# Kernel tuning notes

Hardware: AMD Instinct MI355X
Metric: run time of the kernel (lower is better)

The kernel has to match this reference:

```python
import math
import jax, jax.numpy as jnp
import numpy as np

B, S, D, H = 1, 4096, 1024, 16
HD = D // H


def setup_inputs() -> dict:
    key = jax.random.key(0)
    ks = jax.random.split(key, 11)
    s = 0.02
    inp = {
        "q": jax.random.normal(ks[0], (B, S, D), jnp.float32),
        "k": jax.random.normal(ks[1], (B, S, D), jnp.float32),
        "v": jax.random.normal(ks[2], (B, S, D), jnp.float32),
        # causal boolean mask, broadcastable over [B, H, S, S]
        "mask": jnp.tril(jnp.ones((S, S), jnp.bool_))[None, None],
        "Wq": jax.random.normal(ks[3], (D, D), jnp.float32) * s,
        "bq": jnp.zeros((D,), jnp.float32),
        "Wk": jax.random.normal(ks[4], (D, D), jnp.float32) * s,
        "bk": jnp.zeros((D,), jnp.float32),
        "Wv": jax.random.normal(ks[5], (D, D), jnp.float32) * s,
        "bv": jnp.zeros((D,), jnp.float32),
        "Wo": jax.random.normal(ks[6], (D, D), jnp.float32) * s,
        "bo": jnp.zeros((D,), jnp.float32),
    }
    return inp


def reference(q, k, v, mask, Wq, bq, Wk, bk, Wv, bv, Wo, bo):
    # projections (torch Linear: x @ W.T + b; here W is stored already transposed)
    qp = (q @ Wq + bq).reshape(B, S, H, HD)
    kp = (k @ Wk + bk).reshape(B, S, H, HD)
    vp = (v @ Wv + bv).reshape(B, S, H, HD)
    # scores: [B, H, S, S]
    scores = jnp.einsum("bqhd,bkhd->bhqk", qp, kp) / math.sqrt(HD)
    scores = jnp.where(mask, scores, -jnp.inf)
    attn = jax.nn.softmax(scores, axis=-1)
    # context: [B, H, S, HD] -> [B, S, D]
    ctx = jnp.einsum("bhqk,bkhd->bqhd", attn, vp).reshape(B, S, D)
    return ctx @ Wo + bo
```

## Files before the change

kernel.cpp:

```cpp
#include <hip/hip_runtime.h>
#include <hip/hip_bf16.h>


#define S_LEN 4096
#define D_DIM 1024
#define NHEAD 16
#define HDIM  64

typedef __hip_bfloat16 bf16;
typedef __attribute__((ext_vector_type(8))) short bf16x8v;
typedef __attribute__((ext_vector_type(4))) float f32x4;

#define MFMA16(a, b, c) __builtin_amdgcn_mfma_f32_16x16x32_bf16((a), (b), (c), 0, 0, 0)

__device__ __forceinline__ void async_cp16(const void* g, void* l) {
    __builtin_amdgcn_global_load_lds(
        (const __attribute__((address_space(1))) unsigned int*)g,
        (__attribute__((address_space(3))) unsigned int*)l, 16, 0, 0);
}

__global__ __launch_bounds__(256) void cvt_bf16_k(
    const float* __restrict__ x0, const float* __restrict__ x1,
    const float* __restrict__ x2,
    bf16* __restrict__ y0, bf16* __restrict__ y1, bf16* __restrict__ y2)
{
    const float* x = (blockIdx.z == 0) ? x0 : (blockIdx.z == 1) ? x1 : x2;
    bf16*       y = (blockIdx.z == 0) ? y0 : (blockIdx.z == 1) ? y1 : y2;
    const size_t i = ((size_t)blockIdx.x * 256 + threadIdx.x);
    const float4 v = ((const float4*)x)[i];
    union { bf16 h[4]; short4 s; } u;
    u.h[0] = __float2bfloat16(v.x);
    u.h[1] = __float2bfloat16(v.y);
    u.h[2] = __float2bfloat16(v.z);
    u.h[3] = __float2bfloat16(v.w);
    ((short4*)y)[i] = u.s;
}

__global__ __launch_bounds__(256) void transpose_cvt_k(
    const float* __restrict__ W0, const float* __restrict__ W1,
    const float* __restrict__ W2, const float* __restrict__ W3,
    bf16* __restrict__ T0, bf16* __restrict__ T1,
    bf16* __restrict__ T2, bf16* __restrict__ T3)
{
    const float* W = (blockIdx.z == 0) ? W0 : (blockIdx.z == 1) ? W1
                   : (blockIdx.z == 2) ? W2 : W3;
    bf16*       Wt = (blockIdx.z == 0) ? T0 : (blockIdx.z == 1) ? T1
                   : (blockIdx.z == 2) ? T2 : T3;
    __shared__ float t[32][33];
    const int bx = blockIdx.x << 5, by = blockIdx.y << 5;
    const int tx = threadIdx.x & 31, ty = threadIdx.x >> 5;
#pragma unroll
    for (int i = 0; i < 32; i += 8)
        t[ty + i][tx] = W[(size_t)(by + ty + i) * D_DIM + bx + tx];
    __syncthreads();
#pragma unroll
    for (int i = 0; i < 32; i += 8)
        Wt[(size_t)(bx + ty + i) * D_DIM + by + tx] = __float2bfloat16(t[tx][ty + i]);
}

struct GemmJob {
    const bf16* A; const bf16* Wt; const float* bias; void* out;
    int mode; float scale;
};

__global__ __launch_bounds__(256) void gemm_k(GemmJob j0, GemmJob j1, GemmJob j2)
{
    const GemmJob j = (blockIdx.z == 0) ? j0 : (blockIdx.z == 1) ? j1 : j2;
    const int K = D_DIM;
    const int bn = blockIdx.x << 6;
    const int bm = blockIdx.y << 7;
    const int tid = threadIdx.x;
    const int w = tid >> 6, lane = tid & 63;
    const int col = lane & 15, g = lane >> 4;
    const int wr = (w >> 1) << 6, wc = (w & 1) << 5;

    __shared__ bf16 As[128 * 64];
    __shared__ bf16 Bs[64 * 64];

    f32x4 acc[4][2];
#pragma unroll
    for (int i = 0; i < 4; ++i)
#pragma unroll
        for (int jj = 0; jj < 2; ++jj) acc[i][jj] = (f32x4){0.f, 0.f, 0.f, 0.f};

    for (int kb = 0; kb < K; kb += 64) {
        __syncthreads();
#pragma unroll
        for (int e = 0; e < 4; ++e) {
            const int lin = (e << 8) + tid;
            const int row = lin >> 3, kc = lin & 7;
            async_cp16(j.A + (size_t)(bm + row) * K + kb + (kc << 3), &As[lin << 3]);
        }
#pragma unroll
        for (int e = 0; e < 2; ++e) {
            const int lin = (e << 8) + tid;
            const int row = lin >> 3, kc = lin & 7;
            async_cp16(j.Wt + (size_t)(bn + row) * K + kb + (kc << 3), &Bs[lin << 3]);
        }
        __syncthreads();

#pragma unroll
        for (int s = 0; s < 2; ++s) {
            bf16x8v af[4], bfv[2];
#pragma unroll
            for (int i = 0; i < 4; ++i)
                af[i] = *(const bf16x8v*)&As[((wr + (i << 4) + col) << 6) + (s << 5) + (g << 3)];
#pragma unroll
            for (int jj = 0; jj < 2; ++jj)
                bfv[jj] = *(const bf16x8v*)&Bs[((wc + (jj << 4) + col) << 6) + (s << 5) + (g << 3)];
#pragma unroll
            for (int i = 0; i < 4; ++i)
#pragma unroll
                for (int jj = 0; jj < 2; ++jj)
                    acc[i][jj] = MFMA16(af[i], bfv[jj], acc[i][jj]);
        }
    }

#pragma unroll
    for (int i = 0; i < 4; ++i)
#pragma unroll
    for (int jj = 0; jj < 2; ++jj)
#pragma unroll
    for (int reg = 0; reg < 4; ++reg) {
        const int row = bm + wr + (i << 4) + (g << 2) + reg;
        const int cg  = bn + wc + (jj << 4) + col;
        const float vv = (acc[i][jj][reg] + j.bias[cg]) * j.scale;
        if (j.mode == 0)
            ((bf16*)j.out)[(((size_t)(cg >> 6)) * S_LEN + row) * HDIM + (cg & 63)] =
                __float2bfloat16(vv);
        else if (j.mode == 2)
            ((bf16*)j.out)[((size_t)(cg >> 6) * HDIM + (cg & 63)) * S_LEN + row] =
                __float2bfloat16(vv);
        else
            ((float*)j.out)[(size_t)row * D_DIM + cg] = vv;
    }
}

__global__ __launch_bounds__(256) void attn_mfma_k(
    const bf16* __restrict__ Qp, const bf16* __restrict__ Kp,
    const bf16* __restrict__ Vt, bf16* __restrict__ ctx)
{
    __shared__ bf16 Ks[4096];
    __shared__ bf16 Vs[4096];
    __shared__ bf16 Ps[4][1024];

    const int bid = blockIdx.x;
    const int qb  = 63 - (bid >> 4);
    const int h   = bid & 15;
    const int q0  = qb << 6;
    const int tid = threadIdx.x, w = tid >> 6, lane = tid & 63;
    const int col = lane & 15, g = lane >> 4;

    const bf16* Kh = Kp + (size_t)h * S_LEN * HDIM;
    const bf16* Vh = Vt + (size_t)h * HDIM * S_LEN;

    const size_t qrow_base = ((size_t)h * S_LEN + q0 + (w << 4) + col) * HDIM + (g << 3);
    const bf16x8v qf0 = *(const bf16x8v*)(Qp + qrow_base);
    const bf16x8v qf1 = *(const bf16x8v*)(Qp + qrow_base + 32);

    const int sig_r = (col >> 2) | (((col & 3) ^ (g & 1)) << 2);
    const int pr0 = (((g) << 4) | sig_r) << 3;
    const int pr1 = (((4 + g) << 4) | sig_r) << 3;
    int pw[4][4];
#pragma unroll
    for (int t = 0; t < 4; ++t) {
        const int Gw = (t << 1) + (col >> 3);
#pragma unroll
        for (int reg = 0; reg < 4; ++reg) {
            const int sig = g | (((reg ^ (Gw & 1)) & 3) << 2);
            pw[t][reg] = (((Gw << 4) | sig) << 3) + (col & 7);
        }
    }

    float pl[4] = {0.f, 0.f, 0.f, 0.f};
    f32x4 acco[4];
#pragma unroll
    for (int t = 0; t < 4; ++t) acco[t] = (f32x4){0.f, 0.f, 0.f, 0.f};

    const int nkb = qb + 1;
    for (int kb = 0; kb < nkb; ++kb) {
        const int kk0 = kb << 6;
        __syncthreads();
#pragma unroll
        for (int e = 0; e < 2; ++e) {
            const int lin = (e << 8) + tid;
            const int t = lin >> 7, G = (lin >> 4) & 7, c = lin & 15;
            async_cp16(Kh + (size_t)(kk0 + (t << 4) + c) * HDIM + (G << 3),
                       &Ks[lin << 3]);
            async_cp16(Vh + (size_t)((t << 4) + c) * S_LEN + kk0 + (G << 3),
                       &Vs[lin << 3]);
        }
        __syncthreads();

        f32x4 sa[4];
#pragma unroll
        for (int t = 0; t < 4; ++t) sa[t] = (f32x4){0.f, 0.f, 0.f, 0.f};
#pragma unroll
        for (int t = 0; t < 4; ++t) {
            sa[t] = MFMA16(qf0, *(const bf16x8v*)&Ks[((t << 7) + (g << 4) + col) << 3], sa[t]);
            sa[t] = MFMA16(qf1, *(const bf16x8v*)&Ks[((t << 7) + 64 + (g << 4) + col) << 3], sa[t]);
        }

        const bool lastt = (kb == nkb - 1);
#pragma unroll
        for (int t = 0; t < 4; ++t) {
#pragma unroll
            for (int reg = 0; reg < 4; ++reg) {
                float p;
                if (lastt && (kk0 + (t << 4) + col > q0 + (w << 4) + (g << 2) + reg))
                    p = 0.f;
                else
                    p = __expf(sa[t][reg]);
                pl[reg] += p;
                Ps[w][pw[t][reg]] = __float2bfloat16(p);
            }
        }

        const bf16x8v pf0 = *(const bf16x8v*)&Ps[w][pr0];
        const bf16x8v pf1 = *(const bf16x8v*)&Ps[w][pr1];
#pragma unroll
        for (int t = 0; t < 4; ++t) {
            acco[t] = MFMA16(pf0, *(const bf16x8v*)&Vs[((t << 7) + (g << 4) + col) << 3], acco[t]);
            acco[t] = MFMA16(pf1, *(const bf16x8v*)&Vs[((t << 7) + 64 + (g << 4) + col) << 3], acco[t]);
        }
    }

    float lrow[4];
#pragma unroll
    for (int reg = 0; reg < 4; ++reg) {
        float l = pl[reg];
        l += __shfl_xor(l, 1);
        l += __shfl_xor(l, 2);
        l += __shfl_xor(l, 4);
        l += __shfl_xor(l, 8);
        lrow[reg] = l;
    }

#pragma unroll
    for (int t = 0; t < 4; ++t)
#pragma unroll
        for (int reg = 0; reg < 4; ++reg) {
            const int row = q0 + (w << 4) + (g << 2) + reg;
            ctx[(size_t)row * D_DIM + h * HDIM + (t << 4) + col] =
                __float2bfloat16(acco[t][reg] / lrow[reg]);
        }
}

extern "C" void kernel_launch(void* const* d_in, const int* in_sizes, int n_in,
                              void* d_out, int out_size, void* d_ws, size_t ws_size,
                              hipStream_t stream)
{
    const float* q  = (const float*)d_in[0];
    const float* k  = (const float*)d_in[1];
    const float* v  = (const float*)d_in[2];
    const float* Wq = (const float*)d_in[4];
    const float* bq = (const float*)d_in[5];
    const float* Wk = (const float*)d_in[6];
    const float* bk = (const float*)d_in[7];
    const float* Wv = (const float*)d_in[8];
    const float* bv = (const float*)d_in[9];
    const float* Wo = (const float*)d_in[10];
    const float* bo = (const float*)d_in[11];

    const size_t PE  = (size_t)S_LEN * D_DIM;
    const size_t WTE = (size_t)D_DIM * D_DIM;

    const dim3 tg(32, 32, 4);
    const dim3 gg(D_DIM / 64, S_LEN / 128, 1);
    const dim3 gg3(D_DIM / 64, S_LEN / 128, 3);
    const dim3 cg((unsigned)(PE / 1024), 1, 3);

    if (ws_size >= (size_t)64 * 1024 * 1024) {
        bf16* Qb = (bf16*)d_ws;
        bf16* Kb = Qb + PE;
        bf16* Vb = Kb + PE;
        bf16* Qp = Vb + PE;
        bf16* Kp = Qp + PE;
        bf16* Vt = Kp + PE;
        bf16* Wtq = Vt + PE;
        bf16* Wtk = Wtq + WTE;
        bf16* Wtv = Wtk + WTE;
        bf16* Wto = Wtv + WTE;
        bf16* ctx = Qb;

        transpose_cvt_k<<<tg, 256, 0, stream>>>(Wq, Wk, Wv, Wo, Wtq, Wtk, Wtv, Wto);
        cvt_bf16_k<<<cg, 256, 0, stream>>>(q, k, v, Qb, Kb, Vb);

        GemmJob jq{Qb, Wtq, bq, Qp, 0, 0.125f};
        GemmJob jk{Kb, Wtk, bk, Kp, 0, 1.0f};
        GemmJob jv{Vb, Wtv, bv, Vt, 2, 1.0f};
        gemm_k<<<gg3, 256, 0, stream>>>(jq, jk, jv);

        attn_mfma_k<<<dim3(1024), 256, 0, stream>>>(Qp, Kp, Vt, ctx);

        GemmJob jo{ctx, Wto, bo, d_out, 1, 1.0f};
        gemm_k<<<gg, 256, 0, stream>>>(jo, jo, jo);
    } else {
        bf16* X  = (bf16*)d_ws;
        bf16* Qp = X + PE;
        bf16* Kp = Qp + PE;
        bf16* Vt = Kp + PE;
        bf16* Wtq = Vt + PE;
        bf16* Wtk = Wtq + WTE;
        bf16* Wtv = Wtk + WTE;
        bf16* Wto = Wtv + WTE;

        transpose_cvt_k<<<tg, 256, 0, stream>>>(Wq, Wk, Wv, Wo, Wtq, Wtk, Wtv, Wto);

        const dim3 cg1((unsigned)(PE / 1024), 1, 1);
        cvt_bf16_k<<<cg1, 256, 0, stream>>>(q, q, q, X, X, X);
        GemmJob jq{X, Wtq, bq, Qp, 0, 0.125f};
        gemm_k<<<gg, 256, 0, stream>>>(jq, jq, jq);
        cvt_bf16_k<<<cg1, 256, 0, stream>>>(k, k, k, X, X, X);
        GemmJob jk{X, Wtk, bk, Kp, 0, 1.0f};
        gemm_k<<<gg, 256, 0, stream>>>(jk, jk, jk);
        cvt_bf16_k<<<cg1, 256, 0, stream>>>(v, v, v, X, X, X);
        GemmJob jv{X, Wtv, bv, Vt, 2, 1.0f};
        gemm_k<<<gg, 256, 0, stream>>>(jv, jv, jv);

        attn_mfma_k<<<dim3(1024), 256, 0, stream>>>(Qp, Kp, Vt, X);

        GemmJob jo{X, Wto, bo, d_out, 1, 1.0f};
        gemm_k<<<gg, 256, 0, stream>>>(jo, jo, jo);
    }
}
```

Measured before the change: 324.3 us.

## Enlarge GEMM tiles with swizzled LDS, double-buffer attention K/V, use exp2

```diff
diff --git a/kernel.cpp b/kernel.cpp
--- a/kernel.cpp
+++ b/kernel.cpp
@@ -9,14 +9,20 @@
 
 typedef __hip_bfloat16 bf16;
 typedef __attribute__((ext_vector_type(8))) short bf16x8v;
+typedef __attribute__((ext_vector_type(4))) short bf16x4v;
 typedef __attribute__((ext_vector_type(4))) float f32x4;
 
 #define MFMA16(a, b, c) __builtin_amdgcn_mfma_f32_16x16x32_bf16((a), (b), (c), 0, 0, 0)
+#define LOG2E 1.44269504088896340736f
 
 __device__ __forceinline__ void async_cp16(const void* g, void* l) {
     __builtin_amdgcn_global_load_lds(
         (const __attribute__((address_space(1))) unsigned int*)g,
         (__attribute__((address_space(3))) unsigned int*)l, 16, 0, 0);
+}
+
+__device__ __forceinline__ short bf_bits(float x) {
+    union { bf16 h; short s; } u; u.h = __float2bfloat16(x); return u.s;
 }
 
 __global__ __launch_bounds__(256) void cvt_bf16_k(
@@ -67,51 +73,51 @@
 {
     const GemmJob j = (blockIdx.z == 0) ? j0 : (blockIdx.z == 1) ? j1 : j2;
     const int K = D_DIM;
-    const int bn = blockIdx.x << 6;
+    const int bn = blockIdx.x << 7;
     const int bm = blockIdx.y << 7;
     const int tid = threadIdx.x;
     const int w = tid >> 6, lane = tid & 63;
     const int col = lane & 15, g = lane >> 4;
-    const int wr = (w >> 1) << 6, wc = (w & 1) << 5;
+    const int wr = (w >> 1) << 6, wc = (w & 1) << 6;
 
     __shared__ bf16 As[128 * 64];
-    __shared__ bf16 Bs[64 * 64];
-
-    f32x4 acc[4][2];
+    __shared__ bf16 Bs[128 * 64];
+
+    f32x4 acc[4][4];
 #pragma unroll
     for (int i = 0; i < 4; ++i)
 #pragma unroll
-        for (int jj = 0; jj < 2; ++jj) acc[i][jj] = (f32x4){0.f, 0.f, 0.f, 0.f};
+        for (int jj = 0; jj < 4; ++jj) acc[i][jj] = (f32x4){0.f, 0.f, 0.f, 0.f};
 
     for (int kb = 0; kb < K; kb += 64) {
         __syncthreads();
 #pragma unroll
         for (int e = 0; e < 4; ++e) {
             const int lin = (e << 8) + tid;
-            const int row = lin >> 3, kc = lin & 7;
-            async_cp16(j.A + (size_t)(bm + row) * K + kb + (kc << 3), &As[lin << 3]);
-        }
-#pragma unroll
-        for (int e = 0; e < 2; ++e) {
-            const int lin = (e << 8) + tid;
-            const int row = lin >> 3, kc = lin & 7;
-            async_cp16(j.Wt + (size_t)(bn + row) * K + kb + (kc << 3), &Bs[lin << 3]);
+            const int row = lin >> 3, kcs = lin & 7;
+            const int kcg = kcs ^ (row & 7);
+            async_cp16(j.A  + (size_t)(bm + row) * K + kb + (kcg << 3), &As[lin << 3]);
+            async_cp16(j.Wt + (size_t)(bn + row) * K + kb + (kcg << 3), &Bs[lin << 3]);
         }
         __syncthreads();
 
 #pragma unroll
         for (int s = 0; s < 2; ++s) {
-            bf16x8v af[4], bfv[2];
+            bf16x8v af[4], bfv[4];
+#pragma unroll
+            for (int i = 0; i < 4; ++i) {
+                const int row = wr + (i << 4) + col;
+                af[i] = *(const bf16x8v*)&As[(((row << 3) + (((s << 2) + g) ^ (row & 7)))) << 3];
+            }
+#pragma unroll
+            for (int jj = 0; jj < 4; ++jj) {
+                const int row = wc + (jj << 4) + col;
+                bfv[jj] = *(const bf16x8v*)&Bs[(((row << 3) + (((s << 2) + g) ^ (row & 7)))) << 3];
+            }
 #pragma unroll
             for (int i = 0; i < 4; ++i)
-                af[i] = *(const bf16x8v*)&As[((wr + (i << 4) + col) << 6) + (s << 5) + (g << 3)];
-#pragma unroll
-            for (int jj = 0; jj < 2; ++jj)
-                bfv[jj] = *(const bf16x8v*)&Bs[((wc + (jj << 4) + col) << 6) + (s << 5) + (g << 3)];
-#pragma unroll
-            for (int i = 0; i < 4; ++i)
-#pragma unroll
-                for (int jj = 0; jj < 2; ++jj)
+#pragma unroll
+                for (int jj = 0; jj < 4; ++jj)
                     acc[i][jj] = MFMA16(af[i], bfv[jj], acc[i][jj]);
         }
     }
@@ -119,7 +125,7 @@
 #pragma unroll
     for (int i = 0; i < 4; ++i)
 #pragma unroll
-    for (int jj = 0; jj < 2; ++jj)
+    for (int jj = 0; jj < 4; ++jj)
 #pragma unroll
     for (int reg = 0; reg < 4; ++reg) {
         const int row = bm + wr + (i << 4) + (g << 2) + reg;
@@ -140,8 +146,8 @@
     const bf16* __restrict__ Qp, const bf16* __restrict__ Kp,
     const bf16* __restrict__ Vt, bf16* __restrict__ ctx)
 {
-    __shared__ bf16 Ks[4096];
-    __shared__ bf16 Vs[4096];
+    __shared__ bf16 Ks[2][4096];
+    __shared__ bf16 Vs[2][4096];
     __shared__ bf16 Ps[4][1024];
 
     const int bid = blockIdx.x;
@@ -158,83 +164,85 @@
     const bf16x8v qf0 = *(const bf16x8v*)(Qp + qrow_base);
     const bf16x8v qf1 = *(const bf16x8v*)(Qp + qrow_base + 32);
 
-    const int sig_r = (col >> 2) | (((col & 3) ^ (g & 1)) << 2);
-    const int pr0 = (((g) << 4) | sig_r) << 3;
-    const int pr1 = (((4 + g) << 4) | sig_r) << 3;
-    int pw[4][4];
-#pragma unroll
-    for (int t = 0; t < 4; ++t) {
-        const int Gw = (t << 1) + (col >> 3);
-#pragma unroll
-        for (int reg = 0; reg < 4; ++reg) {
-            const int sig = g | (((reg ^ (Gw & 1)) & 3) << 2);
-            pw[t][reg] = (((Gw << 4) | sig) << 3) + (col & 7);
-        }
-    }
-
-    float pl[4] = {0.f, 0.f, 0.f, 0.f};
+    float pl = 0.f;
     f32x4 acco[4];
 #pragma unroll
     for (int t = 0; t < 4; ++t) acco[t] = (f32x4){0.f, 0.f, 0.f, 0.f};
 
     const int nkb = qb + 1;
+
+#pragma unroll
+    for (int e = 0; e < 2; ++e) {
+        const int lin = (e << 8) + tid;
+        const int t = lin >> 7, G = (lin >> 4) & 7, c = lin & 15;
+        async_cp16(Kh + (size_t)((t << 4) + c) * HDIM + (G << 3), &Ks[0][lin << 3]);
+        async_cp16(Vh + (size_t)((t << 4) + c) * S_LEN + (G << 3), &Vs[0][lin << 3]);
+    }
+
     for (int kb = 0; kb < nkb; ++kb) {
         const int kk0 = kb << 6;
         __syncthreads();
-#pragma unroll
-        for (int e = 0; e < 2; ++e) {
-            const int lin = (e << 8) + tid;
-            const int t = lin >> 7, G = (lin >> 4) & 7, c = lin & 15;
-            async_cp16(Kh + (size_t)(kk0 + (t << 4) + c) * HDIM + (G << 3),
-                       &Ks[lin << 3]);
-            async_cp16(Vh + (size_t)((t << 4) + c) * S_LEN + kk0 + (G << 3),
-                       &Vs[lin << 3]);
-        }
-        __syncthreads();
+        if (kb + 1 < nkb) {
+            const int nk0 = (kb + 1) << 6;
+            const int nb  = (kb + 1) & 1;
+#pragma unroll
+            for (int e = 0; e < 2; ++e) {
+                const int lin = (e << 8) + tid;
+                const int t = lin >> 7, G = (lin >> 4) & 7, c = lin & 15;
+                async_cp16(Kh + (size_t)(nk0 + (t << 4) + c) * HDIM + (G << 3),
+                           &Ks[nb][lin << 3]);
+                async_cp16(Vh + (size_t)((t << 4) + c) * S_LEN + nk0 + (G << 3),
+                           &Vs[nb][lin << 3]);
+            }
+        }
+        const bf16* K0 = Ks[kb & 1];
+        const bf16* V0 = Vs[kb & 1];
 
         f32x4 sa[4];
 #pragma unroll
         for (int t = 0; t < 4; ++t) sa[t] = (f32x4){0.f, 0.f, 0.f, 0.f};
 #pragma unroll
         for (int t = 0; t < 4; ++t) {
-            sa[t] = MFMA16(qf0, *(const bf16x8v*)&Ks[((t << 7) + (g << 4) + col) << 3], sa[t]);
-            sa[t] = MFMA16(qf1, *(const bf16x8v*)&Ks[((t << 7) + 64 + (g << 4) + col) << 3], sa[t]);
+            const bf16x8v kf0 = *(const bf16x8v*)&K0[((t << 7) + (g << 4) + col) << 3];
+            const bf16x8v kf1 = *(const bf16x8v*)&K0[((t << 7) + 64 + (g << 4) + col) << 3];
+            sa[t] = MFMA16(kf0, qf0, sa[t]);
+            sa[t] = MFMA16(kf1, qf1, sa[t]);
         }
 
         const bool lastt = (kb == nkb - 1);
+        const int qq = (w << 4) + col;
 #pragma unroll
         for (int t = 0; t < 4; ++t) {
+            float p[4];
 #pragma unroll
             for (int reg = 0; reg < 4; ++reg) {
-                float p;
-                if (lastt && (kk0 + (t << 4) + col > q0 + (w << 4) + (g << 2) + reg))
-                    p = 0.f;
-                else
-                    p = __expf(sa[t][reg]);
-                pl[reg] += p;
-                Ps[w][pw[t][reg]] = __float2bfloat16(p);
+                const int krel = (t << 4) + (g << 2) + reg;
+                p[reg] = (lastt && krel > qq) ? 0.f
+                       : __builtin_amdgcn_exp2f(sa[t][reg]);
             }
-        }
-
-        const bf16x8v pf0 = *(const bf16x8v*)&Ps[w][pr0];
-        const bf16x8v pf1 = *(const bf16x8v*)&Ps[w][pr1];
+            pl += (p[0] + p[1]) + (p[2] + p[3]);
+            bf16x4v pv = { bf_bits(p[0]), bf_bits(p[1]), bf_bits(p[2]), bf_bits(p[3]) };
+            const int off = (((((t << 1) + (g >> 1)) << 4) + col) << 3) + ((g & 1) << 2);
+            *(bf16x4v*)&Ps[w][off] = pv;
+        }
+
+        const bf16x8v pf0 = *(const bf16x8v*)&Ps[w][((g << 4) + col) << 3];
+        const bf16x8v pf1 = *(const bf16x8v*)&Ps[w][(((4 + g) << 4) + col) << 3];
 #pragma unroll
         for (int t = 0; t < 4; ++t) {
-            acco[t] = MFMA16(pf0, *(const bf16x8v*)&Vs[((t << 7) + (g << 4) + col) << 3], acco[t]);
-            acco[t] = MFMA16(pf1, *(const bf16x8v*)&Vs[((t << 7) + 64 + (g << 4) + col) << 3], acco[t]);
-        }
-    }
-
-    float lrow[4];
-#pragma unroll
-    for (int reg = 0; reg < 4; ++reg) {
-        float l = pl[reg];
-        l += __shfl_xor(l, 1);
-        l += __shfl_xor(l, 2);
-        l += __shfl_xor(l, 4);
-        l += __shfl_xor(l, 8);
-        lrow[reg] = l;
-    }
+            const bf16x8v vf0 = *(const bf16x8v*)&V0[((t << 7) + (g << 4) + col) << 3];
+            const bf16x8v vf1 = *(const bf16x8v*)&V0[((t << 7) + 64 + (g << 4) + col) << 3];
+            acco[t] = MFMA16(pf0, vf0, acco[t]);
+            acco[t] = MFMA16(pf1, vf1, acco[t]);
+        }
+    }
+
+    float l = pl;
+    l += __shfl_xor(l, 16);
+    l += __shfl_xor(l, 32);
+    float lr[4];
+#pragma unroll
+    for (int reg = 0; reg < 4; ++reg) lr[reg] = __shfl(l, (g << 2) + reg);
 
 #pragma unroll
     for (int t = 0; t < 4; ++t)
@@ -242,7 +250,7 @@
         for (int reg = 0; reg < 4; ++reg) {
             const int row = q0 + (w << 4) + (g << 2) + reg;
             ctx[(size_t)row * D_DIM + h * HDIM + (t << 4) + col] =
-                __float2bfloat16(acco[t][reg] / lrow[reg]);
+                __float2bfloat16(acco[t][reg] / lr[reg]);
         }
 }
 
@@ -264,10 +272,11 @@
 
     const size_t PE  = (size_t)S_LEN * D_DIM;
     const size_t WTE = (size_t)D_DIM * D_DIM;
+    const float qscale = 0.125f * LOG2E;
 
     const dim3 tg(32, 32, 4);
-    const dim3 gg(D_DIM / 64, S_LEN / 128, 1);
-    const dim3 gg3(D_DIM / 64, S_LEN / 128, 3);
+    const dim3 gg(D_DIM / 128, S_LEN / 128, 1);
+    const dim3 gg3(D_DIM / 128, S_LEN / 128, 3);
     const dim3 cg((unsigned)(PE / 1024), 1, 3);
 
     if (ws_size >= (size_t)64 * 1024 * 1024) {
@@ -286,7 +295,7 @@
         transpose_cvt_k<<<tg, 256, 0, stream>>>(Wq, Wk, Wv, Wo, Wtq, Wtk, Wtv, Wto);
         cvt_bf16_k<<<cg, 256, 0, stream>>>(q, k, v, Qb, Kb, Vb);
 
-        GemmJob jq{Qb, Wtq, bq, Qp, 0, 0.125f};
+        GemmJob jq{Qb, Wtq, bq, Qp, 0, qscale};
         GemmJob jk{Kb, Wtk, bk, Kp, 0, 1.0f};
         GemmJob jv{Vb, Wtv, bv, Vt, 2, 1.0f};
         gemm_k<<<gg3, 256, 0, stream>>>(jq, jk, jv);
@@ -309,7 +318,7 @@
 
         const dim3 cg1((unsigned)(PE / 1024), 1, 1);
         cvt_bf16_k<<<cg1, 256, 0, stream>>>(q, q, q, X, X, X);
-        GemmJob jq{X, Wtq, bq, Qp, 0, 0.125f};
+        GemmJob jq{X, Wtq, bq, Qp, 0, qscale};
         gemm_k<<<gg, 256, 0, stream>>>(jq, jq, jq);
         cvt_bf16_k<<<cg1, 256, 0, stream>>>(k, k, k, X, X, X);
         GemmJob jk{X, Wtk, bk, Kp, 0, 1.0f};
```

After: 344.4 us. 1.06x slower.
